# Optimization experiments

Measured on AMD Instinct MI355X. Metric: run time of the kernel, lower is better.

The kernel has to match this reference:

```python
import jax, jax.numpy as jnp
import numpy as np

D_MODEL = 1024
N_HEADS = 16
D_HEAD = D_MODEL // N_HEADS
EPS = 1e-5


def setup_inputs() -> dict:
    key = jax.random.key(0)
    ks = jax.random.split(key, 7)
    B, T = 4, 2048
    s = 1.0 / np.sqrt(D_MODEL)
    return {
        "x": jax.random.normal(ks[0], (B, T, D_MODEL), dtype=jnp.float32),
        "ln_g": jnp.ones((D_MODEL,), jnp.float32),
        "ln_b": jnp.zeros((D_MODEL,), jnp.float32),
        "W_qkv": jax.random.normal(ks[1], (D_MODEL, 3 * D_MODEL), jnp.float32) * s,
        "b_qkv": jnp.zeros((3 * D_MODEL,), jnp.float32),
        "W_gate": jax.random.normal(ks[2], (D_MODEL, D_MODEL), jnp.float32) * s,
        "b_gate": jnp.zeros((D_MODEL,), jnp.float32),
        "W_proj": jax.random.normal(ks[3], (D_MODEL, D_MODEL), jnp.float32) * s,
        "b_proj": jnp.zeros((D_MODEL,), jnp.float32),
    }


def _forward(x, ln_g, ln_b, W_qkv, b_qkv, W_gate, b_gate, W_proj, b_proj):
    B, T, D = x.shape
    H, d = N_HEADS, D_HEAD
    # LayerNorm (eps=1e-5, biased variance as in torch)
    mu = jnp.mean(x, axis=-1, keepdims=True)
    var = jnp.mean((x - mu) ** 2, axis=-1, keepdims=True)
    x_norm = (x - mu) * jax.lax.rsqrt(var + EPS) * ln_g + ln_b
    qkv = x_norm @ W_qkv + b_qkv
    q, k, v = jnp.split(qkv, 3, axis=-1)  # each [B,T,D]
    # concept gate uses raw x
    gate = jax.nn.sigmoid(x @ W_gate + b_gate)
    gate = gate / (jnp.mean(gate, axis=-1, keepdims=True) + EPS)
    q = (q * gate).reshape(B, T, H, d)
    k = (k * gate).reshape(B, T, H, d)
    v = v.reshape(B, T, H, d)
    # ReLU^2 feature map in fp32
    q = jax.nn.relu(q.astype(jnp.float32)) ** 2 + EPS
    k = jax.nn.relu(k.astype(jnp.float32)) ** 2 + EPS
    v = v.astype(jnp.float32)
    # causal linear attention via kv recurrence (scan over T, T-major)
    qT = jnp.transpose(q, (1, 0, 2, 3))  # [T,B,H,d]
    kT = jnp.transpose(k, (1, 0, 2, 3))
    vT = jnp.transpose(v, (1, 0, 2, 3))

    def step(carry, inp):
        kv_s, k_s = carry  # [B,H,d,d], [B,H,d]
        q_t, k_t, v_t = inp  # [B,H,d]
        kv_s = kv_s + k_t[..., :, None] * v_t[..., None, :]
        k_s = k_s + k_t
        num = jnp.einsum('bhd,bhdm->bhm', q_t, kv_s)
        den = jnp.einsum('bhd,bhd->bh', q_t, k_s)[..., None] + EPS
        return (kv_s, k_s), num / den

    init = (jnp.zeros((B, H, d, d), jnp.float32), jnp.zeros((B, H, d), jnp.float32))
    _, outT = jax.lax.scan(step, init, (qT, kT, vT))  # [T,B,H,d]
    out = jnp.transpose(outT, (1, 0, 2, 3)).astype(x.dtype).reshape(B, T, D)
    return out @ W_proj + b_proj


def reference(x, ln_g, ln_b, W_qkv, b_qkv, W_gate, b_gate, W_proj, b_proj):
    return _forward(x, ln_g, ln_b, W_qkv, b_qkv, W_gate, b_gate, W_proj, b_proj)
```

## Files before the change

### kernel.cpp

```cpp
#include <hip/hip_runtime.h>
#include <math.h>

#define TOK 8192
#define DM 1024
#define EPSF 1e-5f

typedef __attribute__((ext_vector_type(8))) short short8;
typedef __attribute__((ext_vector_type(4))) float f32x4;

static __device__ __forceinline__ ushort f2bf(float f) {
  unsigned u = __float_as_uint(f);
  unsigned r = (u + 0x7fffu + ((u >> 16) & 1u)) >> 16;
  return (ushort)r;
}
static __device__ __forceinline__ float bf2f(ushort u) {
  return __uint_as_float((unsigned)u << 16);
}

static __device__ __forceinline__ void gload_lds16(const ushort* g, ushort* l) {
  __builtin_amdgcn_global_load_lds((const __attribute__((address_space(1))) void*)g,
                                   (__attribute__((address_space(3))) void*)l, 16, 0, 0);
}

static __device__ __forceinline__ int cswz(int row) {
  return (((row & 7) ^ ((row >> 3) & 7)) << 3);
}

static __device__ __forceinline__ int2 xcd_remap(int nx) {
  int bid = blockIdx.y * nx + blockIdx.x;
  int nwg = nx * gridDim.y;
  int cpx = nwg >> 3;
  int id = (bid & 7) * cpx + (bid >> 3);
  return make_int2(id % nx, id / nx);
}

__global__ __launch_bounds__(256) void lncvt_k(const float* __restrict__ x,
                                               const float* __restrict__ g,
                                               const float* __restrict__ b,
                                               ushort* __restrict__ x_b,
                                               ushort* __restrict__ xn_b) {
  __shared__ float red[8];
  int row = blockIdx.x;
  const float4* xr = (const float4*)(x + (size_t)row * DM);
  float4 v = xr[threadIdx.x];
  ushort4 xb4;
  xb4.x = f2bf(v.x); xb4.y = f2bf(v.y); xb4.z = f2bf(v.z); xb4.w = f2bf(v.w);
  ((ushort4*)(x_b + (size_t)row * DM))[threadIdx.x] = xb4;
  float s = v.x + v.y + v.z + v.w;
#pragma unroll
  for (int o = 32; o > 0; o >>= 1) s += __shfl_down(s, o, 64);
  int lane = threadIdx.x & 63, w = threadIdx.x >> 6;
  if (lane == 0) red[w] = s;
  __syncthreads();
  float mu = (red[0] + red[1] + red[2] + red[3]) * (1.0f / DM);
  float dx = v.x - mu, dy = v.y - mu, dz = v.z - mu, dw = v.w - mu;
  float ss = dx * dx + dy * dy + dz * dz + dw * dw;
#pragma unroll
  for (int o = 32; o > 0; o >>= 1) ss += __shfl_down(ss, o, 64);
  if (lane == 0) red[4 + w] = ss;
  __syncthreads();
  float var = (red[4] + red[5] + red[6] + red[7]) * (1.0f / DM);
  float rstd = rsqrtf(var + EPSF);
  float4 gg = ((const float4*)g)[threadIdx.x];
  float4 bb = ((const float4*)b)[threadIdx.x];
  ushort4 o4;
  o4.x = f2bf(dx * rstd * gg.x + bb.x);
  o4.y = f2bf(dy * rstd * gg.y + bb.y);
  o4.z = f2bf(dz * rstd * gg.z + bb.z);
  o4.w = f2bf(dw * rstd * gg.w + bb.w);
  ((ushort4*)(xn_b + (size_t)row * DM))[threadIdx.x] = o4;
}

__global__ __launch_bounds__(256) void tconv_k(const float* __restrict__ W,
                                               ushort* __restrict__ Wt, int K, int N) {
  __shared__ ushort tile[32][33];
  int k0 = blockIdx.y * 32, n0 = blockIdx.x * 32;
  int tx = threadIdx.x & 31, ty = threadIdx.x >> 5;
#pragma unroll
  for (int i = 0; i < 4; i++) {
    int k = ty + i * 8;
    tile[k][tx] = f2bf(W[(size_t)(k0 + k) * N + n0 + tx]);
  }
  __syncthreads();
#pragma unroll
  for (int i = 0; i < 4; i++) {
    int n = ty + i * 8;
    Wt[(size_t)(n0 + n) * K + k0 + tx] = tile[tx][n];
  }
}

__global__ __launch_bounds__(256) void rowinv_k(const ushort* __restrict__ gate_b,
                                                float* __restrict__ ginv) {
  int row = blockIdx.x * 4 + (threadIdx.x >> 6);
  int l = threadIdx.x & 63;
  const short8* gr = (const short8*)(gate_b + (size_t)row * DM);
  short8 g0 = gr[l * 2], g1 = gr[l * 2 + 1];
  float s = 0.f;
#pragma unroll
  for (int j = 0; j < 8; j++) s += bf2f((ushort)g0[j]) + bf2f((ushort)g1[j]);
#pragma unroll
  for (int o = 1; o < 64; o <<= 1) s += __shfl_xor(s, o, 64);
  if (l == 0) ginv[row] = 1.0f / (s * (1.0f / DM) + EPSF);
}

#define BM 128
#define BN 128
#define BK 64
__global__ __launch_bounds__(256) void gemm_bf16_k(
    const ushort* __restrict__ A, const ushort* __restrict__ Bt,
    const float* __restrict__ bias, float* __restrict__ Cf,
    ushort* __restrict__ Cb, int ldc, int K, int mode) {
  __shared__ __align__(16) ushort As[BM * BK];
  __shared__ __align__(16) ushort Bs[BN * BK];
  int tid = threadIdx.x, lane = tid & 63, w = tid >> 6;
  int2 bxy = xcd_remap(gridDim.x);
  int m0 = bxy.y * BM, n0 = bxy.x * BN;
  int wr = w >> 1, wc = w & 1;
  f32x4 acc[4][4] = {};
  for (int k0 = 0; k0 < K; k0 += BK) {
#pragma unroll
    for (int j = 0; j < 4; j++) {
      int lu = (w * 4 + j) * 64 + lane;
      int r = lu >> 3;
      int kb = (lu & 7) ^ (r & 7);
      gload_lds16(A + (size_t)(m0 + r) * K + k0 + kb * 8, &As[(w * 4 + j) * 512]);
      gload_lds16(Bt + (size_t)(n0 + r) * K + k0 + kb * 8, &Bs[(w * 4 + j) * 512]);
    }
    __syncthreads();
#pragma unroll
    for (int ks = 0; ks < 2; ks++) {
      short8 af[4], bfr[4];
      int kq = ks * 4 + (lane >> 4);
#pragma unroll
      for (int f = 0; f < 4; f++) {
        int ra = wr * 64 + f * 16 + (lane & 15);
        af[f] = *(const short8*)&As[(ra * 8 + (kq ^ (ra & 7))) * 8];
        int rb = wc * 64 + f * 16 + (lane & 15);
        bfr[f] = *(const short8*)&Bs[(rb * 8 + (kq ^ (rb & 7))) * 8];
      }
#pragma unroll
      for (int i = 0; i < 4; i++)
#pragma unroll
        for (int j2 = 0; j2 < 4; j2++)
          acc[i][j2] = __builtin_amdgcn_mfma_f32_16x16x32_bf16(af[i], bfr[j2], acc[i][j2], 0, 0, 0);
    }
    __syncthreads();
  }
#pragma unroll
  for (int i = 0; i < 4; i++) {
#pragma unroll
    for (int j2 = 0; j2 < 4; j2++) {
      int col = n0 + wc * 64 + j2 * 16 + (lane & 15);
      float bv = bias[col];
#pragma unroll
      for (int r = 0; r < 4; r++) {
        int row = m0 + wr * 64 + i * 16 + (lane >> 4) * 4 + r;
        float v = acc[i][j2][r] + bv;
        if (mode == 2) {
          v = 1.0f / (1.0f + expf(-v));
          Cb[(size_t)row * ldc + col] = f2bf(v);
        } else {
          Cf[(size_t)row * ldc + col] = v;
        }
      }
    }
  }
}

__global__ __launch_bounds__(256) void gemm_qkv_k(
    const ushort* __restrict__ A, const ushort* __restrict__ Bt,
    const float* __restrict__ bias, const ushort* __restrict__ gate_b,
    const float* __restrict__ ginv,
    ushort* __restrict__ qb, ushort* __restrict__ kb,
    ushort* __restrict__ kt, ushort* __restrict__ vt, int K) {
  __shared__ __align__(16) ushort sh[16896];
  __shared__ float ginvs[128];
  ushort* As = sh;
  ushort* Bs = sh + BM * BK;
  int tid = threadIdx.x, lane = tid & 63, w = tid >> 6;
  int2 bxy = xcd_remap(gridDim.x);
  int m0 = bxy.y * BM, n0 = bxy.x * BN;
  int wr = w >> 1, wc = w & 1;
  f32x4 acc[4][4] = {};
  for (int k0 = 0; k0 < K; k0 += BK) {
#pragma unroll
    for (int j = 0; j < 4; j++) {
      int lu = (w * 4 + j) * 64 + lane;
      int r = lu >> 3;
      int kb2 = (lu & 7) ^ (r & 7);
      gload_lds16(A + (size_t)(m0 + r) * K + k0 + kb2 * 8, &As[(w * 4 + j) * 512]);
      gload_lds16(Bt + (size_t)(n0 + r) * K + k0 + kb2 * 8, &Bs[(w * 4 + j) * 512]);
    }
    __syncthreads();
#pragma unroll
    for (int ks = 0; ks < 2; ks++) {
      short8 af[4], bfr[4];
      int kq = ks * 4 + (lane >> 4);
#pragma unroll
      for (int f = 0; f < 4; f++) {
        int ra = wr * 64 + f * 16 + (lane & 15);
        af[f] = *(const short8*)&As[(ra * 8 + (kq ^ (ra & 7))) * 8];
        int rb = wc * 64 + f * 16 + (lane & 15);
        bfr[f] = *(const short8*)&Bs[(rb * 8 + (kq ^ (rb & 7))) * 8];
      }
#pragma unroll
      for (int i = 0; i < 4; i++)
#pragma unroll
        for (int j2 = 0; j2 < 4; j2++)
          acc[i][j2] = __builtin_amdgcn_mfma_f32_16x16x32_bf16(af[i], bfr[j2], acc[i][j2], 0, 0, 0);
    }
    __syncthreads();
  }
  int region = n0 >> 10;
  int n0b = n0 & 1023;
  int h0 = n0b >> 6;
  if (region < 2) {
    if (tid < 128) ginvs[tid] = ginv[m0 + tid];
#pragma unroll
    for (int it = 0; it < 8; it++) {
      int e = it * 256 + tid;
      int row = e >> 4, ch = e & 15;
      *(short8*)&sh[row * 132 + ch * 8] =
          *(const short8*)&gate_b[(size_t)(m0 + row) * DM + n0b + ch * 8];
    }
    __syncthreads();
#pragma unroll
    for (int i = 0; i < 4; i++) {
#pragma unroll
      for (int j2 = 0; j2 < 4; j2++) {
        int cl = wc * 64 + j2 * 16 + (lane & 15);
        float bv = bias[n0 + cl];
        int rl0 = wr * 64 + i * 16 + (lane >> 4) * 4;
#pragma unroll
        for (int r = 0; r < 4; r++) {
          float gv = bf2f(sh[(rl0 + r) * 132 + cl]) * ginvs[rl0 + r];
          float v = (acc[i][j2][r] + bv) * gv;
          v = fmaxf(v, 0.0f);
          acc[i][j2][r] = v * v + EPSF;
        }
      }
    }
    __syncthreads();
  } else {
#pragma unroll
    for (int i = 0; i < 4; i++)
#pragma unroll
      for (int j2 = 0; j2 < 4; j2++) {
        int cl = wc * 64 + j2 * 16 + (lane & 15);
        float bv = bias[n0 + cl];
#pragma unroll
        for (int r = 0; r < 4; r++) acc[i][j2][r] += bv;
      }
  }
#pragma unroll
  for (int i = 0; i < 4; i++) {
#pragma unroll
    for (int j2 = 0; j2 < 4; j2++) {
      int cl = wc * 64 + j2 * 16 + (lane & 15);
      int rl0 = wr * 64 + i * 16 + (lane >> 4) * 4;
#pragma unroll
      for (int r = 0; r < 4; r++) {
        int row = rl0 + r;
        sh[row * 128 + (cl ^ cswz(row))] = f2bf(acc[i][j2][r]);
      }
    }
  }
  __syncthreads();
  if (region < 2) {
    ushort* dstRM = (region == 0) ? qb : kb;
#pragma unroll
    for (int it = 0; it < 8; it++) {
      int e = it * 256 + tid;
      int row = e >> 4, ch = e & 15;
      short8 val = *(const short8*)&sh[row * 128 + ((ch * 8) ^ cswz(row))];
      int tglob = m0 + row;
      size_t bh2 = (size_t)(tglob >> 11) * 16 + h0 + (ch >> 3);
      *(short8*)&dstRM[(bh2 * 2048 + (tglob & 2047)) * 64 + (ch & 7) * 8] = val;
    }
  }
  if (region >= 1) {
    ushort* dstT = (region == 1) ? kt : vt;
#pragma unroll
    for (int it = 0; it < 8; it++) {
      int e = it * 256 + tid;
      int tch = e & 15, dkrow = e >> 4;
      short8 val;
#pragma unroll
      for (int j = 0; j < 8; j++) {
        int row = tch * 8 + j;
        val[j] = (short)sh[row * 128 + (dkrow ^ cswz(row))];
      }
      int tglob0 = m0 + tch * 8;
      size_t bh2 = (size_t)(tglob0 >> 11) * 16 + h0 + (dkrow >> 6);
      *(short8*)&dstT[(bh2 * 64 + (dkrow & 63)) * 2048 + (tglob0 & 2047)] = val;
    }
  }
}

__global__ __launch_bounds__(256) void chunkpfx_k(const ushort* __restrict__ kt,
                                                  const ushort* __restrict__ vt,
                                                  ushort* __restrict__ KVb,
                                                  float* __restrict__ ksum) {
  int dvs = blockIdx.x, bh = blockIdx.y;
  int tid = threadIdx.x, l = tid & 63, w = tid >> 6;
  int lr = l & 15, lg = l >> 4;
  const ushort* vT = vt + ((size_t)bh * 64 + dvs * 16 + lr) * 2048;
  const ushort* kT = kt + ((size_t)bh * 64 + w * 16 + lr) * 2048;
  f32x4 run = {0.f, 0.f, 0.f, 0.f};
  float runks = 0.0f;
  short8 a0 = *(const short8*)&vT[lg * 8];
  short8 a1 = *(const short8*)&vT[32 + lg * 8];
  short8 b0 = *(const short8*)&kT[lg * 8];
  short8 b1 = *(const short8*)&kT[32 + lg * 8];
  for (int c = 0; c < 32; c++) {
    ushort* dst = KVb + ((size_t)bh * 32 + c) * 4096 +
                  (size_t)(dvs * 16 + lg * 4) * 64 + w * 16 + lr;
    dst[0] = f2bf(run[0]); dst[64] = f2bf(run[1]);
    dst[128] = f2bf(run[2]); dst[192] = f2bf(run[3]);
    if (dvs == 0) {
      float s = 0.f;
#pragma unroll
      for (int j = 0; j < 8; j++) s += bf2f((ushort)b0[j]) + bf2f((ushort)b1[j]);
      s += __shfl_xor(s, 16, 64);
      s += __shfl_xor(s, 32, 64);
      if (l < 16) ksum[((size_t)bh * 32 + c) * 64 + w * 16 + l] = runks;
      runks += s;
    }
    int cn = (c + 1) & 31;
    short8 na0 = *(const short8*)&vT[cn * 64 + lg * 8];
    short8 na1 = *(const short8*)&vT[cn * 64 + 32 + lg * 8];
    short8 nb0 = *(const short8*)&kT[cn * 64 + lg * 8];
    short8 nb1 = *(const short8*)&kT[cn * 64 + 32 + lg * 8];
    run = __builtin_amdgcn_mfma_f32_16x16x32_bf16(a0, b0, run, 0, 0, 0);
    run = __builtin_amdgcn_mfma_f32_16x16x32_bf16(a1, b1, run, 0, 0, 0);
    a0 = na0; a1 = na1; b0 = nb0; b1 = nb1;
  }
}

__global__ __launch_bounds__(256) void attn_k(
    const ushort* __restrict__ qb, const ushort* __restrict__ kb,
    const ushort* __restrict__ vt, const ushort* __restrict__ KVb,
    const float* __restrict__ ks, ushort* __restrict__ attnout) {
  int c = blockIdx.x, bh = blockIdx.y;
  int b = bh >> 4, h = bh & 15;
  const ushort* qB = qb + ((size_t)bh * 2048 + (size_t)c * 64) * 64;
  const ushort* kB = kb + ((size_t)bh * 2048 + (size_t)c * 64) * 64;
  const ushort* vT = vt + (size_t)bh * 64 * 2048 + (size_t)c * 64;
  const ushort* kvB = KVb + ((size_t)bh * 32 + c) * 4096;
  const float* ksP = ks + ((size_t)bh * 32 + c) * 64;
  __shared__ __align__(16) char SL[64 * 128];
  __shared__ float denp[4][64];
  __shared__ float den2p[4][64];
  __shared__ float invden[64];
  int tid = threadIdx.x, l = tid & 63, w = tid >> 6;
  int lr = l & 15, lg = l >> 4;
  {
    short8 q0 = *(const short8*)&qB[(size_t)l * 64 + w * 16];
    short8 q1 = *(const short8*)&qB[(size_t)l * 64 + w * 16 + 8];
    float d2 = 0.0f;
#pragma unroll
    for (int j = 0; j < 8; j++) {
      d2 += bf2f((ushort)q0[j]) * ksP[w * 16 + j];
      d2 += bf2f((ushort)q1[j]) * ksP[w * 16 + 8 + j];
    }
    den2p[w][l] = d2;
  }
#pragma unroll
  for (int n = 0; n < 4; n++) {
    f32x4 sa = {0.f, 0.f, 0.f, 0.f};
#pragma unroll
    for (int g = 0; g < 2; g++) {
      short8 a = *(const short8*)&kB[(size_t)(w * 16 + lr) * 64 + g * 32 + lg * 8];
      short8 bq = *(const short8*)&qB[(size_t)(n * 16 + lr) * 64 + g * 32 + lg * 8];
      sa = __builtin_amdgcn_mfma_f32_16x16x32_bf16(a, bq, sa, 0, 0, 0);
    }
    int t = n * 16 + lr;
    int s0 = w * 16 + lg * 4;
    float dsum = 0.0f;
    ushort sb[4];
#pragma unroll
    for (int r = 0; r < 4; r++) {
      float v = (s0 + r <= t) ? sa[r] : 0.0f;
      dsum += v;
      sb[r] = f2bf(v);
    }
    dsum += __shfl_xor(dsum, 16, 64);
    dsum += __shfl_xor(dsum, 32, 64);
    if (l < 16) denp[w][n * 16 + l] = dsum;
    int u = (s0 >> 3) ^ (t & 7);
    uint2 p;
    p.x = sb[0] | ((unsigned)sb[1] << 16);
    p.y = sb[2] | ((unsigned)sb[3] << 16);
    *(uint2*)&SL[t * 128 + u * 16 + (s0 & 7) * 2] = p;
  }
  __syncthreads();
  if (tid < 64) {
    float den = denp[0][tid] + denp[1][tid] + denp[2][tid] + denp[3][tid] +
                den2p[0][tid] + den2p[1][tid] + den2p[2][tid] + den2p[3][tid] + EPSF;
    invden[tid] = 1.0f / den;
  }
  __syncthreads();
#pragma unroll
  for (int n = 0; n < 4; n++) {
    f32x4 oa = {0.f, 0.f, 0.f, 0.f};
#pragma unroll
    for (int g = 0; g < 2; g++) {
      short8 a = *(const short8*)&kvB[(size_t)(w * 16 + lr) * 64 + g * 32 + lg * 8];
      short8 bq = *(const short8*)&qB[(size_t)(n * 16 + lr) * 64 + g * 32 + lg * 8];
      oa = __builtin_amdgcn_mfma_f32_16x16x32_bf16(a, bq, oa, 0, 0, 0);
    }
    int t = n * 16 + lr;
#pragma unroll
    for (int g = 0; g < 2; g++) {
      short8 a = *(const short8*)&vT[(size_t)(w * 16 + lr) * 2048 + g * 32 + lg * 8];
      int u = (g * 4 + lg) ^ (t & 7);
      short8 bs = *(const short8*)&SL[t * 128 + u * 16];
      oa = __builtin_amdgcn_mfma_f32_16x16x32_bf16(a, bs, oa, 0, 0, 0);
    }
    float iv = invden[t];
    ushort ob[4];
#pragma unroll
    for (int r = 0; r < 4; r++) ob[r] = f2bf(oa[r] * iv);
    size_t tok = (size_t)b * 2048 + (size_t)c * 64 + t;
    uint2 p;
    p.x = ob[0] | ((unsigned)ob[1] << 16);
    p.y = ob[2] | ((unsigned)ob[3] << 16);
    *(uint2*)&attnout[tok * 1024 + h * 64 + w * 16 + lg * 4] = p;
  }
}

extern "C" void kernel_launch(void* const* d_in, const int* in_sizes, int n_in,
                              void* d_out, int out_size, void* d_ws, size_t ws_size,
                              hipStream_t stream) {
  const float* x      = (const float*)d_in[0];
  const float* ln_g   = (const float*)d_in[1];
  const float* ln_b   = (const float*)d_in[2];
  const float* W_qkv  = (const float*)d_in[3];
  const float* b_qkv  = (const float*)d_in[4];
  const float* W_gate = (const float*)d_in[5];
  const float* b_gate = (const float*)d_in[6];
  const float* W_proj = (const float*)d_in[7];
  const float* b_proj = (const float*)d_in[8];
  float* out = (float*)d_out;

  char* wsb = (char*)d_ws;
  const size_t TD = (size_t)TOK * DM;
  const size_t SLOT = TD * 2;
  ushort* x_b     = (ushort*)(wsb + 0 * SLOT);
  ushort* attnout = (ushort*)(wsb + 0 * SLOT);
  ushort* xn_b    = (ushort*)(wsb + 1 * SLOT);
  ushort* qb      = (ushort*)(wsb + 2 * SLOT);
  ushort* kb      = (ushort*)(wsb + 3 * SLOT);
  ushort* kt      = (ushort*)(wsb + 4 * SLOT);
  ushort* vt      = (ushort*)(wsb + 5 * SLOT);
  ushort* gate_b  = (ushort*)(wsb + 6 * SLOT);
  ushort* Wt_gate = (ushort*)(wsb + 8 * SLOT);
  ushort* Wt_qkv  = (ushort*)(wsb + 8 * SLOT);
  ushort* KVb     = (ushort*)(wsb + 8 * SLOT);
  ushort* Wt_proj = (ushort*)(wsb + 9 * SLOT);
  float*  ksum    = (float*)(wsb + 9 * SLOT + 8 * 1024 * 1024);
  float*  ginv    = (float*)(wsb + 9 * SLOT + 12 * 1024 * 1024);

  lncvt_k<<<TOK, 256, 0, stream>>>(x, ln_g, ln_b, x_b, xn_b);
  tconv_k<<<dim3(DM / 32, DM / 32), 256, 0, stream>>>(W_gate, Wt_gate, DM, DM);
  gemm_bf16_k<<<dim3(DM / BN, TOK / BM), 256, 0, stream>>>(x_b, Wt_gate, b_gate, nullptr,
                                                           gate_b, DM, DM, 2);
  rowinv_k<<<TOK / 4, 256, 0, stream>>>(gate_b, ginv);
  tconv_k<<<dim3(3 * DM / 32, DM / 32), 256, 0, stream>>>(W_qkv, Wt_qkv, DM, 3 * DM);
  gemm_qkv_k<<<dim3(3 * DM / BN, TOK / BM), 256, 0, stream>>>(xn_b, Wt_qkv, b_qkv, gate_b,
                                                              ginv, qb, kb, kt, vt, DM);
  chunkpfx_k<<<dim3(4, 64), 256, 0, stream>>>(kt, vt, KVb, ksum);
  tconv_k<<<dim3(DM / 32, DM / 32), 256, 0, stream>>>(W_proj, Wt_proj, DM, DM);
  attn_k<<<dim3(32, 64), 256, 0, stream>>>(qb, kb, vt, KVb, ksum, attnout);
  gemm_bf16_k<<<dim3(DM / BN, TOK / BM), 256, 0, stream>>>(attnout, Wt_proj, b_proj, out,
                                                           nullptr, DM, DM, 0);
}
```

Baseline: 211.7 us.

## Rewrite GEMMs as 256x128 double-buffered 512-thread kernels with async prefetch

```diff
diff --git a/kernel.cpp b/kernel.cpp
--- a/kernel.cpp
+++ b/kernel.cpp
@@ -26,12 +26,10 @@
   return (((row & 7) ^ ((row >> 3) & 7)) << 3);
 }
 
-static __device__ __forceinline__ int2 xcd_remap(int nx) {
-  int bid = blockIdx.y * nx + blockIdx.x;
-  int nwg = nx * gridDim.y;
-  int cpx = nwg >> 3;
-  int id = (bid & 7) * cpx + (bid >> 3);
-  return make_int2(id % nx, id / nx);
+static __device__ __forceinline__ int swz_off(int r, int kq) {
+  int sr = r & 15;
+  int gp = ((kq >> 1) & 1) ^ ((sr >> 3) & 1);
+  return (((r >> 4) * 2 + (kq >> 2)) << 9) | (sr << 5) | (gp << 4) | ((kq & 1) << 3);
 }
 
 __global__ __launch_bounds__(256) void lncvt_k(const float* __restrict__ x,
@@ -103,59 +101,93 @@
   if (l == 0) ginv[row] = 1.0f / (s * (1.0f / DM) + EPSF);
 }
 
-#define BM 128
-#define BN 128
-#define BK 64
-__global__ __launch_bounds__(256) void gemm_bf16_k(
+
+static __device__ __forceinline__ void stage_tile(
+    const ushort* __restrict__ A, const ushort* __restrict__ Bt,
+    int m0, int n0, int k0, ushort* bufA, ushort* bufB, int w, int lane) {
+#pragma unroll
+  for (int j = 0; j < 4; j++) {
+    int lu = (w * 4 + j) * 64 + lane;
+    int r = ((lu >> 7) << 4) | ((lu >> 2) & 15);
+    int kq = (((lu >> 6) & 1) << 2) | ((((lu >> 1) ^ (lu >> 5)) & 1) << 1) | (lu & 1);
+    gload_lds16(A + (size_t)(m0 + r) * 1024 + k0 + kq * 8, bufA + (w * 4 + j) * 512);
+  }
+#pragma unroll
+  for (int j = 0; j < 2; j++) {
+    int lu = (w * 2 + j) * 64 + lane;
+    int r = ((lu >> 7) << 4) | ((lu >> 2) & 15);
+    int kq = (((lu >> 6) & 1) << 2) | ((((lu >> 1) ^ (lu >> 5)) & 1) << 1) | (lu & 1);
+    gload_lds16(Bt + (size_t)(n0 + r) * 1024 + k0 + kq * 8, bufB + (w * 2 + j) * 512);
+  }
+}
+
+static __device__ __forceinline__ void tile_mfma(const ushort* bufA, const ushort* bufB,
+                                                 int wm, int wn, int lane,
+                                                 f32x4 acc[8][2]) {
+#pragma unroll
+  for (int ks = 0; ks < 2; ks++) {
+    int kq = ks * 4 + (lane >> 4);
+    short8 af[8], bfv[2];
+#pragma unroll
+    for (int nf = 0; nf < 2; nf++)
+      bfv[nf] = *(const short8*)&bufB[swz_off(wn * 32 + nf * 16 + (lane & 15), kq)];
+#pragma unroll
+    for (int mf = 0; mf < 8; mf++)
+      af[mf] = *(const short8*)&bufA[swz_off(wm * 128 + mf * 16 + (lane & 15), kq)];
+    __builtin_amdgcn_s_setprio(1);
+#pragma unroll
+    for (int mf = 0; mf < 8; mf++)
+#pragma unroll
+      for (int nf = 0; nf < 2; nf++)
+        acc[mf][nf] = __builtin_amdgcn_mfma_f32_16x16x32_bf16(af[mf], bfv[nf], acc[mf][nf], 0, 0, 0);
+    __builtin_amdgcn_s_setprio(0);
+  }
+}
+
+#define GEMM_MAINLOOP(A_, B_, m0_, n0_)                                        \
+  ushort* bA0 = sh;                                                            \
+  ushort* bA1 = sh + 16384;                                                    \
+  ushort* bB0 = sh + 32768;                                                    \
+  ushort* bB1 = sh + 40960;                                                    \
+  f32x4 acc[8][2] = {};                                                        \
+  stage_tile(A_, B_, m0_, n0_, 0, bA0, bB0, w, lane);                          \
+  stage_tile(A_, B_, m0_, n0_, 64, bA1, bB1, w, lane);                         \
+  _Pragma("unroll 2")                                                          \
+  for (int t = 0; t < 16; t++) {                                               \
+    if (t < 15) { asm volatile("s_waitcnt vmcnt(6)" ::: "memory"); }           \
+    else        { asm volatile("s_waitcnt vmcnt(0)" ::: "memory"); }           \
+    __builtin_amdgcn_sched_barrier(0);                                         \
+    __builtin_amdgcn_s_barrier();                                              \
+    __builtin_amdgcn_sched_barrier(0);                                         \
+    tile_mfma((t & 1) ? bA1 : bA0, (t & 1) ? bB1 : bB0, wm, wn, lane, acc);    \
+    asm volatile("s_waitcnt lgkmcnt(0)" ::: "memory");                         \
+    __builtin_amdgcn_sched_barrier(0);                                         \
+    __builtin_amdgcn_s_barrier();                                              \
+    __builtin_amdgcn_sched_barrier(0);                                         \
+    if (t < 14)                                                                \
+      stage_tile(A_, B_, m0_, n0_, (t + 2) * 64, (t & 1) ? bA1 : bA0,          \
+                 (t & 1) ? bB1 : bB0, w, lane);                                \
+  }
+
+__global__ __launch_bounds__(512, 2) void gemm256_k(
     const ushort* __restrict__ A, const ushort* __restrict__ Bt,
     const float* __restrict__ bias, float* __restrict__ Cf,
-    ushort* __restrict__ Cb, int ldc, int K, int mode) {
-  __shared__ __align__(16) ushort As[BM * BK];
-  __shared__ __align__(16) ushort Bs[BN * BK];
+    ushort* __restrict__ Cb, int ldc, int mode) {
+  extern __shared__ __align__(16) ushort sh[];
   int tid = threadIdx.x, lane = tid & 63, w = tid >> 6;
-  int2 bxy = xcd_remap(gridDim.x);
-  int m0 = bxy.y * BM, n0 = bxy.x * BN;
-  int wr = w >> 1, wc = w & 1;
-  f32x4 acc[4][4] = {};
-  for (int k0 = 0; k0 < K; k0 += BK) {
-#pragma unroll
-    for (int j = 0; j < 4; j++) {
-      int lu = (w * 4 + j) * 64 + lane;
-      int r = lu >> 3;
-      int kb = (lu & 7) ^ (r & 7);
-      gload_lds16(A + (size_t)(m0 + r) * K + k0 + kb * 8, &As[(w * 4 + j) * 512]);
-      gload_lds16(Bt + (size_t)(n0 + r) * K + k0 + kb * 8, &Bs[(w * 4 + j) * 512]);
-    }
-    __syncthreads();
-#pragma unroll
-    for (int ks = 0; ks < 2; ks++) {
-      short8 af[4], bfr[4];
-      int kq = ks * 4 + (lane >> 4);
-#pragma unroll
-      for (int f = 0; f < 4; f++) {
-        int ra = wr * 64 + f * 16 + (lane & 15);
-        af[f] = *(const short8*)&As[(ra * 8 + (kq ^ (ra & 7))) * 8];
-        int rb = wc * 64 + f * 16 + (lane & 15);
-        bfr[f] = *(const short8*)&Bs[(rb * 8 + (kq ^ (rb & 7))) * 8];
-      }
-#pragma unroll
-      for (int i = 0; i < 4; i++)
-#pragma unroll
-        for (int j2 = 0; j2 < 4; j2++)
-          acc[i][j2] = __builtin_amdgcn_mfma_f32_16x16x32_bf16(af[i], bfr[j2], acc[i][j2], 0, 0, 0);
-    }
-    __syncthreads();
-  }
-#pragma unroll
-  for (int i = 0; i < 4; i++) {
-#pragma unroll
-    for (int j2 = 0; j2 < 4; j2++) {
-      int col = n0 + wc * 64 + j2 * 16 + (lane & 15);
+  int wm = w >> 2, wn = w & 3;
+  int m0 = blockIdx.y * 256, n0 = blockIdx.x * 128;
+  GEMM_MAINLOOP(A, Bt, m0, n0)
+#pragma unroll
+  for (int mf = 0; mf < 8; mf++) {
+#pragma unroll
+    for (int nf = 0; nf < 2; nf++) {
+      int col = n0 + wn * 32 + nf * 16 + (lane & 15);
       float bv = bias[col];
 #pragma unroll
       for (int r = 0; r < 4; r++) {
-        int row = m0 + wr * 64 + i * 16 + (lane >> 4) * 4 + r;
-        float v = acc[i][j2][r] + bv;
+        int row = m0 + wm * 128 + mf * 16 + (lane >> 4) * 4 + r;
+        float v = acc[mf][nf][r] + bv;
         if (mode == 2) {
           v = 1.0f / (1.0f + expf(-v));
           Cb[(size_t)row * ldc + col] = f2bf(v);
@@ -167,110 +199,77 @@
   }
 }
 
-__global__ __launch_bounds__(256) void gemm_qkv_k(
+__global__ __launch_bounds__(512, 2) void gemm256_qkv_k(
     const ushort* __restrict__ A, const ushort* __restrict__ Bt,
     const float* __restrict__ bias, const ushort* __restrict__ gate_b,
     const float* __restrict__ ginv,
     ushort* __restrict__ qb, ushort* __restrict__ kb,
-    ushort* __restrict__ kt, ushort* __restrict__ vt, int K) {
-  __shared__ __align__(16) ushort sh[16896];
-  __shared__ float ginvs[128];
-  ushort* As = sh;
-  ushort* Bs = sh + BM * BK;
+    ushort* __restrict__ kt, ushort* __restrict__ vt) {
+  extern __shared__ __align__(16) ushort sh[];
   int tid = threadIdx.x, lane = tid & 63, w = tid >> 6;
-  int2 bxy = xcd_remap(gridDim.x);
-  int m0 = bxy.y * BM, n0 = bxy.x * BN;
-  int wr = w >> 1, wc = w & 1;
-  f32x4 acc[4][4] = {};
-  for (int k0 = 0; k0 < K; k0 += BK) {
-#pragma unroll
-    for (int j = 0; j < 4; j++) {
-      int lu = (w * 4 + j) * 64 + lane;
-      int r = lu >> 3;
-      int kb2 = (lu & 7) ^ (r & 7);
-      gload_lds16(A + (size_t)(m0 + r) * K + k0 + kb2 * 8, &As[(w * 4 + j) * 512]);
-      gload_lds16(Bt + (size_t)(n0 + r) * K + k0 + kb2 * 8, &Bs[(w * 4 + j) * 512]);
-    }
-    __syncthreads();
-#pragma unroll
-    for (int ks = 0; ks < 2; ks++) {
-      short8 af[4], bfr[4];
-      int kq = ks * 4 + (lane >> 4);
-#pragma unroll
-      for (int f = 0; f < 4; f++) {
-        int ra = wr * 64 + f * 16 + (lane & 15);
-        af[f] = *(const short8*)&As[(ra * 8 + (kq ^ (ra & 7))) * 8];
-        int rb = wc * 64 + f * 16 + (lane & 15);
-        bfr[f] = *(const short8*)&Bs[(rb * 8 + (kq ^ (rb & 7))) * 8];
-      }
-#pragma unroll
-      for (int i = 0; i < 4; i++)
-#pragma unroll
-        for (int j2 = 0; j2 < 4; j2++)
-          acc[i][j2] = __builtin_amdgcn_mfma_f32_16x16x32_bf16(af[i], bfr[j2], acc[i][j2], 0, 0, 0);
-    }
-    __syncthreads();
-  }
+  int wm = w >> 2, wn = w & 3;
+  int m0 = blockIdx.y * 256, n0 = blockIdx.x * 128;
+  GEMM_MAINLOOP(A, Bt, m0, n0)
   int region = n0 >> 10;
   int n0b = n0 & 1023;
   int h0 = n0b >> 6;
   if (region < 2) {
-    if (tid < 128) ginvs[tid] = ginv[m0 + tid];
+    float* ginvs = (float*)(sh + 37888);
+    if (tid < 256) ginvs[tid] = ginv[m0 + tid];
 #pragma unroll
     for (int it = 0; it < 8; it++) {
-      int e = it * 256 + tid;
+      int e = it * 512 + tid;
       int row = e >> 4, ch = e & 15;
-      *(short8*)&sh[row * 132 + ch * 8] =
+      *(short8*)&sh[row * 136 + ch * 8] =
           *(const short8*)&gate_b[(size_t)(m0 + row) * DM + n0b + ch * 8];
     }
     __syncthreads();
 #pragma unroll
-    for (int i = 0; i < 4; i++) {
-#pragma unroll
-      for (int j2 = 0; j2 < 4; j2++) {
-        int cl = wc * 64 + j2 * 16 + (lane & 15);
+    for (int mf = 0; mf < 8; mf++) {
+#pragma unroll
+      for (int nf = 0; nf < 2; nf++) {
+        int cl = wn * 32 + nf * 16 + (lane & 15);
         float bv = bias[n0 + cl];
-        int rl0 = wr * 64 + i * 16 + (lane >> 4) * 4;
+        int rl0 = wm * 128 + mf * 16 + (lane >> 4) * 4;
 #pragma unroll
         for (int r = 0; r < 4; r++) {
-          float gv = bf2f(sh[(rl0 + r) * 132 + cl]) * ginvs[rl0 + r];
-          float v = (acc[i][j2][r] + bv) * gv;
+          float gv = bf2f(sh[(rl0 + r) * 136 + cl]) * ginvs[rl0 + r];
+          float v = (acc[mf][nf][r] + bv) * gv;
           v = fmaxf(v, 0.0f);
-          acc[i][j2][r] = v * v + EPSF;
+          acc[mf][nf][r] = v * v + EPSF;
         }
       }
     }
     __syncthreads();
   } else {
 #pragma unroll
-    for (int i = 0; i < 4; i++)
-#pragma unroll
-      for (int j2 = 0; j2 < 4; j2++) {
-        int cl = wc * 64 + j2 * 16 + (lane & 15);
+    for (int mf = 0; mf < 8; mf++)
+#pragma unroll
+      for (int nf = 0; nf < 2; nf++) {
+        int cl = wn * 32 + nf * 16 + (lane & 15);
         float bv = bias[n0 + cl];
 #pragma unroll
-        for (int r = 0; r < 4; r++) acc[i][j2][r] += bv;
+        for (int r = 0; r < 4; r++) acc[mf][nf][r] += bv;
       }
   }
 #pragma unroll
-  for (int i = 0; i < 4; i++) {
-#pragma unroll
-    for (int j2 = 0; j2 < 4; j2++) {
-      int cl = wc * 64 + j2 * 16 + (lane & 15);
-      int rl0 = wr * 64 + i * 16 + (lane >> 4) * 4;
+  for (int mf = 0; mf < 8; mf++)
+#pragma unroll
+    for (int nf = 0; nf < 2; nf++) {
+      int cl = wn * 32 + nf * 16 + (lane & 15);
+      int rl0 = wm * 128 + mf * 16 + (lane >> 4) * 4;
 #pragma unroll
       for (int r = 0; r < 4; r++) {
         int row = rl0 + r;
-        sh[row * 128 + (cl ^ cswz(row))] = f2bf(acc[i][j2][r]);
+        sh[row * 128 + (cl ^ cswz(row))] = f2bf(acc[mf][nf][r]);
       }
     }
-  }
   __syncthreads();
   if (region < 2) {
     ushort* dstRM = (region == 0) ? qb : kb;
 #pragma unroll
     for (int it = 0; it < 8; it++) {
-      int e = it * 256 + tid;
+      int e = it * 512 + tid;
       int row = e >> 4, ch = e & 15;
       short8 val = *(const short8*)&sh[row * 128 + ((ch * 8) ^ cswz(row))];
       int tglob = m0 + row;
@@ -282,8 +281,8 @@
     ushort* dstT = (region == 1) ? kt : vt;
 #pragma unroll
     for (int it = 0; it < 8; it++) {
-      int e = it * 256 + tid;
-      int tch = e & 15, dkrow = e >> 4;
+      int e = it * 512 + tid;
+      int dkrow = e >> 5, tch = e & 31;
       short8 val;
 #pragma unroll
       for (int j = 0; j < 8; j++) {
@@ -301,11 +300,13 @@
                                                   const ushort* __restrict__ vt,
                                                   ushort* __restrict__ KVb,
                                                   float* __restrict__ ksum) {
-  int dvs = blockIdx.x, bh = blockIdx.y;
+  int bid = blockIdx.x;
+  int bh = (bid & 7) | ((bid >> 5) << 3);
+  int dvs = (bid >> 3) & 3;
   int tid = threadIdx.x, l = tid & 63, w = tid >> 6;
-  int lr = l & 15, lg = l >> 4;
-  const ushort* vT = vt + ((size_t)bh * 64 + dvs * 16 + lr) * 2048;
-  const ushort* kT = kt + ((size_t)bh * 64 + w * 16 + lr) * 2048;
+  int lg = l >> 4;
+  const ushort* vT = vt + ((size_t)bh * 64 + dvs * 16 + (l & 15)) * 2048;
+  const ushort* kT = kt + ((size_t)bh * 64 + w * 16 + (l & 15)) * 2048;
   f32x4 run = {0.f, 0.f, 0.f, 0.f};
   float runks = 0.0f;
   short8 a0 = *(const short8*)&vT[lg * 8];
@@ -314,7 +315,7 @@
   short8 b1 = *(const short8*)&kT[32 + lg * 8];
   for (int c = 0; c < 32; c++) {
     ushort* dst = KVb + ((size_t)bh * 32 + c) * 4096 +
-                  (size_t)(dvs * 16 + lg * 4) * 64 + w * 16 + lr;
+                  (size_t)(dvs * 16 + lg * 4) * 64 + w * 16 + (l & 15);
     dst[0] = f2bf(run[0]); dst[64] = f2bf(run[1]);
     dst[128] = f2bf(run[2]); dst[192] = f2bf(run[3]);
     if (dvs == 0) {
@@ -461,17 +462,23 @@
   float*  ksum    = (float*)(wsb + 9 * SLOT + 8 * 1024 * 1024);
   float*  ginv    = (float*)(wsb + 9 * SLOT + 12 * 1024 * 1024);
 
+  const int SHB = 96 * 1024;
+  (void)hipFuncSetAttribute((const void*)gemm256_k,
+                            hipFuncAttributeMaxDynamicSharedMemorySize, SHB);
+  (void)hipFuncSetAttribute((const void*)gemm256_qkv_k,
+                            hipFuncAttributeMaxDynamicSharedMemorySize, SHB);
+
   lncvt_k<<<TOK, 256, 0, stream>>>(x, ln_g, ln_b, x_b, xn_b);
   tconv_k<<<dim3(DM / 32, DM / 32), 256, 0, stream>>>(W_gate, Wt_gate, DM, DM);
-  gemm_bf16_k<<<dim3(DM / BN, TOK / BM), 256, 0, stream>>>(x_b, Wt_gate, b_gate, nullptr,
-                                                           gate_b, DM, DM, 2);
+  gemm256_k<<<dim3(DM / 128, TOK / 256), 512, SHB, stream>>>(x_b, Wt_gate, b_gate,
+                                                             nullptr, gate_b, DM, 2);
   rowinv_k<<<TOK / 4, 256, 0, stream>>>(gate_b, ginv);
   tconv_k<<<dim3(3 * DM / 32, DM / 32), 256, 0, stream>>>(W_qkv, Wt_qkv, DM, 3 * DM);
-  gemm_qkv_k<<<dim3(3 * DM / BN, TOK / BM), 256, 0, stream>>>(xn_b, Wt_qkv, b_qkv, gate_b,
-                                                              ginv, qb, kb, kt, vt, DM);
-  chunkpfx_k<<<dim3(4, 64), 256, 0, stream>>>(kt, vt, KVb, ksum);
+  gemm256_qkv_k<<<dim3(3 * DM / 128, TOK / 256), 512, SHB, stream>>>(
+      xn_b, Wt_qkv, b_qkv, gate_b, ginv, qb, kb, kt, vt);
+  chunkpfx_k<<<256, 256, 0, stream>>>(kt, vt, KVb, ksum);
   tconv_k<<<dim3(DM / 32, DM / 32), 256, 0, stream>>>(W_proj, Wt_proj, DM, DM);
   attn_k<<<dim3(32, 64), 256, 0, stream>>>(qb, kb, vt, KVb, ksum, attnout);
-  gemm_bf16_k<<<dim3(DM / BN, TOK / BM), 256, 0, stream>>>(attnout, Wt_proj, b_proj, out,
-                                                           nullptr, DM, DM, 0);
-}
+  gemm256_k<<<dim3(DM / 128, TOK / 256), 512, SHB, stream>>>(attnout, Wt_proj, b_proj,
+                                                             out, nullptr, DM, 0);
+}
```

Result: no change. 213.2 us (+0.7%).
